# Kernel optimization log

Hardware: AMD Instinct MI355X
Metric: run time of the kernel (lower is better)

## Reference

```python
import jax, jax.numpy as jnp
import numpy as np

N_NODES = 10000
N_EDGES = 640000
D_FEAT = 128


def setup_inputs() -> dict:
    key = jax.random.key(0)
    k1, k2, k3, k4 = jax.random.split(key, 4)
    edge_feat = jax.random.normal(k1, (N_EDGES, D_FEAT), dtype=jnp.float32)
    node_feat = jax.random.normal(k2, (N_NODES, D_FEAT), dtype=jnp.float32)
    recv_idx = jax.random.randint(k3, (N_EDGES,), 0, N_NODES, dtype=jnp.int64 if jax.config.jax_enable_x64 else jnp.int32)
    W = jax.random.normal(k4, (2 * D_FEAT, D_FEAT), dtype=jnp.float32) * (1.0 / np.sqrt(2 * D_FEAT))
    b = jnp.zeros((D_FEAT,), dtype=jnp.float32)
    return {"edge_feat": edge_feat, "node_feat": node_feat, "recv_idx": recv_idx, "W": W, "b": b}


def reference(edge_feat, node_feat, recv_idx, W, b):
    # Unsorted segment sum: scatter-add edge features into receiver nodes. [E,d] -> [N,d]
    n_nodes = node_feat.shape[0]
    agg = jax.ops.segment_sum(edge_feat, recv_idx, num_segments=n_nodes)
    # Concat node features with aggregated received-edge features. [N, 2d]
    collected = jnp.concatenate([node_feat, agg], axis=-1)
    # node_model: Linear(2d -> d)
    return collected @ W + b
```

## Files before the change

kernel.cpp:

```cpp
#include <hip/hip_runtime.h>

#define N_NODES 10000
#define N_EDGES 640000
#define D_FEAT 128

#define WS_COUNTS 0
#define WS_START  16384
#define WS_CURSOR 32768
#define WS_SORTED 49152
#define WS_INTS_NEEDED (WS_SORTED + N_EDGES)

__global__ void zero_counts_kernel(int* __restrict__ counts) {
    int i = blockIdx.x * blockDim.x + threadIdx.x;
    if (i < N_NODES) counts[i] = 0;
}

__global__ void hist_kernel(const int* __restrict__ recv, int* __restrict__ counts) {
    int e = blockIdx.x * blockDim.x + threadIdx.x;
    if (e < N_EDGES) atomicAdd(&counts[recv[e]], 1);
}

__global__ __launch_bounds__(1024) void prefix_kernel(const int* __restrict__ counts,
                                                      int* __restrict__ start,
                                                      int* __restrict__ cursor) {
    __shared__ int wsum[16];
    __shared__ int carry_s;
    const int tid  = threadIdx.x;
    const int lane = tid & 63;
    const int wave = tid >> 6;
    if (tid == 0) carry_s = 0;
    __syncthreads();
    for (int base = 0; base < N_NODES; base += 1024) {
        const int idx = base + tid;
        const int v = (idx < N_NODES) ? counts[idx] : 0;
        int x = v;
        #pragma unroll
        for (int off = 1; off < 64; off <<= 1) {
            int t = __shfl_up(x, off, 64);
            if (lane >= off) x += t;
        }
        if (lane == 63) wsum[wave] = x;
        __syncthreads();
        if (wave == 0) {
            int ws = (lane < 16) ? wsum[lane] : 0;
            #pragma unroll
            for (int off = 1; off < 16; off <<= 1) {
                int t = __shfl_up(ws, off, 64);
                if (lane >= off) ws += t;
            }
            if (lane < 16) wsum[lane] = ws;
        }
        __syncthreads();
        const int carry   = carry_s;
        const int waveoff = (wave == 0) ? 0 : wsum[wave - 1];
        const int excl    = carry + waveoff + x - v;
        if (idx < N_NODES) { start[idx] = excl; cursor[idx] = excl; }
        __syncthreads();
        if (tid == 1023) carry_s = carry + wsum[15];
    }
    if (tid == 0) start[N_NODES] = N_EDGES;
}

__global__ void reorder_kernel(const int* __restrict__ recv,
                               int* __restrict__ cursor,
                               int* __restrict__ sorted_eid) {
    int e = blockIdx.x * blockDim.x + threadIdx.x;
    if (e < N_EDGES) {
        int pos = atomicAdd(&cursor[recv[e]], 1);
        sorted_eid[pos] = e;
    }
}

#define GW 8
__global__ __launch_bounds__(256) void gather_kernel(
        const float4* __restrict__ edge_feat4,
        const int* __restrict__ sorted_eid,
        const int* __restrict__ start,
        float4* __restrict__ agg4) {
    __shared__ float4 red[GW][32];
    const int n   = blockIdx.x;
    const int tid = threadIdx.x;
    const int l   = tid & 31;
    const int w   = tid >> 5;
    const int s = start[n];
    const int e = start[n + 1];
    float4 acc = {0.f, 0.f, 0.f, 0.f};
    for (int i = s + w; i < e; i += GW) {
        const long eid = sorted_eid[i];
        const float4 v = edge_feat4[eid * 32 + l];
        acc.x += v.x; acc.y += v.y; acc.z += v.z; acc.w += v.w;
    }
    red[w][l] = acc;
    __syncthreads();
    if (w == 0) {
        float4 r = red[0][l];
        #pragma unroll
        for (int k = 1; k < GW; ++k) {
            const float4 t = red[k][l];
            r.x += t.x; r.y += t.y; r.z += t.z; r.w += t.w;
        }
        agg4[(long)n * 32 + l] = r;
    }
}

#define NT 16
__global__ __launch_bounds__(128) void gemm_kernel(
        const float* __restrict__ node_feat,
        const float* __restrict__ agg,
        const float* __restrict__ W,
        const float* __restrict__ b,
        float* __restrict__ out) {
    __shared__ float coll[NT][2 * D_FEAT];
    const int n0 = blockIdx.x * NT;
    const int j  = threadIdx.x;

    #pragma unroll
    for (int i = 0; i < NT; ++i) {
        coll[i][j]          = node_feat[(long)(n0 + i) * D_FEAT + j];
        coll[i][D_FEAT + j] = agg[(long)(n0 + i) * D_FEAT + j];
    }
    __syncthreads();

    float acc[NT];
    const float bias = b[j];
    #pragma unroll
    for (int i = 0; i < NT; ++i) acc[i] = bias;

    for (int k = 0; k < 2 * D_FEAT; k += 4) {
        const float w0 = W[(long)(k + 0) * D_FEAT + j];
        const float w1 = W[(long)(k + 1) * D_FEAT + j];
        const float w2 = W[(long)(k + 2) * D_FEAT + j];
        const float w3 = W[(long)(k + 3) * D_FEAT + j];
        #pragma unroll
        for (int i = 0; i < NT; ++i) {
            const float4 c = *(const float4*)&coll[i][k];
            acc[i] += c.x * w0 + c.y * w1 + c.z * w2 + c.w * w3;
        }
    }

    #pragma unroll
    for (int i = 0; i < NT; ++i)
        out[(long)(n0 + i) * D_FEAT + j] = acc[i];
}

extern "C" void kernel_launch(void* const* d_in, const int* in_sizes, int n_in,
                              void* d_out, int out_size, void* d_ws, size_t ws_size,
                              hipStream_t stream) {
    const float* edge_feat = (const float*)d_in[0];
    const float* node_feat = (const float*)d_in[1];
    const int*   recv      = (const int*)d_in[2];
    const float* W         = (const float*)d_in[3];
    const float* b         = (const float*)d_in[4];
    float* out = (float*)d_out;
    float* agg = out;

    int* wsi    = (int*)d_ws;
    int* counts = wsi + WS_COUNTS;
    int* startp = wsi + WS_START;
    int* cursor = wsi + WS_CURSOR;
    int* sorted = wsi + WS_SORTED;

    zero_counts_kernel<<<(N_NODES + 255) / 256, 256, 0, stream>>>(counts);
    hist_kernel<<<(N_EDGES + 255) / 256, 256, 0, stream>>>(recv, counts);
    prefix_kernel<<<1, 1024, 0, stream>>>(counts, startp, cursor);
    reorder_kernel<<<(N_EDGES + 255) / 256, 256, 0, stream>>>(recv, cursor, sorted);
    gather_kernel<<<N_NODES, 256, 0, stream>>>(
        (const float4*)edge_feat, sorted, startp, (float4*)agg);
    gemm_kernel<<<N_NODES / NT, 128, 0, stream>>>(node_feat, agg, W, b, out);
}
```

Baseline: 577.9 us.

## Parallelize prefix scan, vectorize histogram/reorder, prefetch gather, tile GEMM

The single-block prefix scan becomes a three-kernel multi-block scan. Histogram and reorder now read four receiver indices per thread as int4. The gather uses 16 waves per node and prefetches the next sorted edge id while the current row loads. The GEMM becomes a 64x64 register-tiled SGEMM with shared-memory A/B tiles, and agg moves from the output buffer into workspace. These target the serial scan latency and the low-reuse GEMM, at the cost of extra launches and more workspace.

```diff
diff --git a/kernel.cpp b/kernel.cpp
--- a/kernel.cpp
+++ b/kernel.cpp
@@ -5,74 +5,100 @@
 #define D_FEAT 128
 
 #define WS_COUNTS 0
+#define WS_BSUM   10240
+#define WS_BOFF   10304
 #define WS_START  16384
 #define WS_CURSOR 32768
 #define WS_SORTED 49152
-#define WS_INTS_NEEDED (WS_SORTED + N_EDGES)
+#define WS_AGG    689152
+
+#define NPB 40
 
 __global__ void zero_counts_kernel(int* __restrict__ counts) {
     int i = blockIdx.x * blockDim.x + threadIdx.x;
     if (i < N_NODES) counts[i] = 0;
 }
 
-__global__ void hist_kernel(const int* __restrict__ recv, int* __restrict__ counts) {
-    int e = blockIdx.x * blockDim.x + threadIdx.x;
-    if (e < N_EDGES) atomicAdd(&counts[recv[e]], 1);
-}
-
-__global__ __launch_bounds__(1024) void prefix_kernel(const int* __restrict__ counts,
+__global__ void hist_kernel(const int4* __restrict__ recv4, int* __restrict__ counts) {
+    int i = blockIdx.x * blockDim.x + threadIdx.x;
+    if (i < N_EDGES / 4) {
+        const int4 r = recv4[i];
+        atomicAdd(&counts[r.x], 1);
+        atomicAdd(&counts[r.y], 1);
+        atomicAdd(&counts[r.z], 1);
+        atomicAdd(&counts[r.w], 1);
+    }
+}
+
+__global__ __launch_bounds__(256) void prefix1_kernel(const int* __restrict__ counts,
+                                                      int* __restrict__ bsum) {
+    __shared__ int wsum[4];
+    const int tid = threadIdx.x;
+    const int idx = blockIdx.x * 256 + tid;
+    int x = (idx < N_NODES) ? counts[idx] : 0;
+    #pragma unroll
+    for (int off = 32; off >= 1; off >>= 1) x += __shfl_down(x, off, 64);
+    if ((tid & 63) == 0) wsum[tid >> 6] = x;
+    __syncthreads();
+    if (tid == 0) bsum[blockIdx.x] = wsum[0] + wsum[1] + wsum[2] + wsum[3];
+}
+
+__global__ void prefix2_kernel(const int* __restrict__ bsum,
+                               int* __restrict__ boff,
+                               int* __restrict__ start) {
+    const int lane = threadIdx.x;
+    const int v = (lane < NPB) ? bsum[lane] : 0;
+    int x = v;
+    #pragma unroll
+    for (int off = 1; off < 64; off <<= 1) {
+        int t = __shfl_up(x, off, 64);
+        if (lane >= off) x += t;
+    }
+    if (lane < NPB) boff[lane] = x - v;
+    if (lane == 0) start[N_NODES] = N_EDGES;
+}
+
+__global__ __launch_bounds__(256) void prefix3_kernel(const int* __restrict__ counts,
+                                                      const int* __restrict__ boff,
                                                       int* __restrict__ start,
                                                       int* __restrict__ cursor) {
-    __shared__ int wsum[16];
-    __shared__ int carry_s;
+    __shared__ int wsum[4];
     const int tid  = threadIdx.x;
+    const int idx  = blockIdx.x * 256 + tid;
     const int lane = tid & 63;
     const int wave = tid >> 6;
-    if (tid == 0) carry_s = 0;
+    const int v = (idx < N_NODES) ? counts[idx] : 0;
+    int x = v;
+    #pragma unroll
+    for (int off = 1; off < 64; off <<= 1) {
+        int t = __shfl_up(x, off, 64);
+        if (lane >= off) x += t;
+    }
+    if (lane == 63) wsum[wave] = x;
     __syncthreads();
-    for (int base = 0; base < N_NODES; base += 1024) {
-        const int idx = base + tid;
-        const int v = (idx < N_NODES) ? counts[idx] : 0;
-        int x = v;
-        #pragma unroll
-        for (int off = 1; off < 64; off <<= 1) {
-            int t = __shfl_up(x, off, 64);
-            if (lane >= off) x += t;
-        }
-        if (lane == 63) wsum[wave] = x;
-        __syncthreads();
-        if (wave == 0) {
-            int ws = (lane < 16) ? wsum[lane] : 0;
-            #pragma unroll
-            for (int off = 1; off < 16; off <<= 1) {
-                int t = __shfl_up(ws, off, 64);
-                if (lane >= off) ws += t;
-            }
-            if (lane < 16) wsum[lane] = ws;
-        }
-        __syncthreads();
-        const int carry   = carry_s;
-        const int waveoff = (wave == 0) ? 0 : wsum[wave - 1];
-        const int excl    = carry + waveoff + x - v;
-        if (idx < N_NODES) { start[idx] = excl; cursor[idx] = excl; }
-        __syncthreads();
-        if (tid == 1023) carry_s = carry + wsum[15];
-    }
-    if (tid == 0) start[N_NODES] = N_EDGES;
-}
-
-__global__ void reorder_kernel(const int* __restrict__ recv,
+    int woff = 0;
+    #pragma unroll
+    for (int k = 0; k < 3; ++k) woff += (k < wave) ? wsum[k] : 0;
+    const int excl = boff[blockIdx.x] + woff + x - v;
+    if (idx < N_NODES) { start[idx] = excl; cursor[idx] = excl; }
+}
+
+__global__ void reorder_kernel(const int4* __restrict__ recv4,
                                int* __restrict__ cursor,
                                int* __restrict__ sorted_eid) {
-    int e = blockIdx.x * blockDim.x + threadIdx.x;
-    if (e < N_EDGES) {
-        int pos = atomicAdd(&cursor[recv[e]], 1);
-        sorted_eid[pos] = e;
-    }
-}
-
-#define GW 8
-__global__ __launch_bounds__(256) void gather_kernel(
+    int i = blockIdx.x * blockDim.x + threadIdx.x;
+    if (i < N_EDGES / 4) {
+        const int4 r = recv4[i];
+        const int e = i * 4;
+        sorted_eid[atomicAdd(&cursor[r.x], 1)] = e + 0;
+        sorted_eid[atomicAdd(&cursor[r.y], 1)] = e + 1;
+        sorted_eid[atomicAdd(&cursor[r.z], 1)] = e + 2;
+        sorted_eid[atomicAdd(&cursor[r.w], 1)] = e + 3;
+    }
+}
+
+#define GW 16
+__global__ __launch_bounds__(512) void gather_kernel(
         const float4* __restrict__ edge_feat4,
         const int* __restrict__ sorted_eid,
         const int* __restrict__ start,
@@ -85,62 +111,104 @@
     const int s = start[n];
     const int e = start[n + 1];
     float4 acc = {0.f, 0.f, 0.f, 0.f};
-    for (int i = s + w; i < e; i += GW) {
-        const long eid = sorted_eid[i];
-        const float4 v = edge_feat4[eid * 32 + l];
-        acc.x += v.x; acc.y += v.y; acc.z += v.z; acc.w += v.w;
+    int i = s + w;
+    if (i < e) {
+        int eid = sorted_eid[i];
+        while (true) {
+            const int inext = i + GW;
+            const int eid_next = (inext < e) ? sorted_eid[inext] : 0;
+            const float4 v = edge_feat4[(long)eid * 32 + l];
+            acc.x += v.x; acc.y += v.y; acc.z += v.z; acc.w += v.w;
+            i = inext;
+            if (i >= e) break;
+            eid = eid_next;
+        }
     }
     red[w][l] = acc;
     __syncthreads();
     if (w == 0) {
         float4 r = red[0][l];
         #pragma unroll
-        for (int k = 1; k < GW; ++k) {
-            const float4 t = red[k][l];
+        for (int g = 1; g < GW; ++g) {
+            const float4 t = red[g][l];
             r.x += t.x; r.y += t.y; r.z += t.z; r.w += t.w;
         }
         agg4[(long)n * 32 + l] = r;
     }
 }
 
-#define NT 16
-__global__ __launch_bounds__(128) void gemm_kernel(
+__global__ __launch_bounds__(256) void gemm_kernel(
         const float* __restrict__ node_feat,
         const float* __restrict__ agg,
         const float* __restrict__ W,
         const float* __restrict__ b,
         float* __restrict__ out) {
-    __shared__ float coll[NT][2 * D_FEAT];
-    const int n0 = blockIdx.x * NT;
-    const int j  = threadIdx.x;
-
-    #pragma unroll
-    for (int i = 0; i < NT; ++i) {
-        coll[i][j]          = node_feat[(long)(n0 + i) * D_FEAT + j];
-        coll[i][D_FEAT + j] = agg[(long)(n0 + i) * D_FEAT + j];
-    }
-    __syncthreads();
-
-    float acc[NT];
-    const float bias = b[j];
-    #pragma unroll
-    for (int i = 0; i < NT; ++i) acc[i] = bias;
-
-    for (int k = 0; k < 2 * D_FEAT; k += 4) {
-        const float w0 = W[(long)(k + 0) * D_FEAT + j];
-        const float w1 = W[(long)(k + 1) * D_FEAT + j];
-        const float w2 = W[(long)(k + 2) * D_FEAT + j];
-        const float w3 = W[(long)(k + 3) * D_FEAT + j];
+    __shared__ __align__(16) float As[32][68];
+    __shared__ __align__(16) float Bs[32][64];
+    const int tid = threadIdx.x;
+    const int tx = tid & 15;
+    const int ty = tid >> 4;
+    const int m0 = blockIdx.x * 64;
+    const int n0 = blockIdx.y * 64;
+
+    float acc[4][4] = {};
+
+    for (int kt = 0; kt < 2 * D_FEAT; kt += 32) {
+        const float* src = (kt < D_FEAT) ? (node_feat + kt) : (agg + (kt - D_FEAT));
+        {
+            const int r  = tid >> 3;
+            const int c4 = tid & 7;
+            #pragma unroll
+            for (int p = 0; p < 2; ++p) {
+                int row = m0 + p * 32 + r;
+                row = (row < N_NODES) ? row : (N_NODES - 1);
+                const float4 a4 = *(const float4*)(src + (long)row * D_FEAT + c4 * 4);
+                As[c4 * 4 + 0][p * 32 + r] = a4.x;
+                As[c4 * 4 + 1][p * 32 + r] = a4.y;
+                As[c4 * 4 + 2][p * 32 + r] = a4.z;
+                As[c4 * 4 + 3][p * 32 + r] = a4.w;
+            }
+        }
+        {
+            const int r  = tid >> 4;
+            const int c4 = tid & 15;
+            #pragma unroll
+            for (int p = 0; p < 2; ++p) {
+                const int row = kt + p * 16 + r;
+                *(float4*)&Bs[p * 16 + r][c4 * 4] =
+                    *(const float4*)(W + (long)row * D_FEAT + n0 + c4 * 4);
+            }
+        }
+        __syncthreads();
         #pragma unroll
-        for (int i = 0; i < NT; ++i) {
-            const float4 c = *(const float4*)&coll[i][k];
-            acc[i] += c.x * w0 + c.y * w1 + c.z * w2 + c.w * w3;
-        }
-    }
-
-    #pragma unroll
-    for (int i = 0; i < NT; ++i)
-        out[(long)(n0 + i) * D_FEAT + j] = acc[i];
+        for (int kk = 0; kk < 32; ++kk) {
+            const float4 a4 = *(const float4*)&As[kk][ty * 4];
+            const float4 b4 = *(const float4*)&Bs[kk][tx * 4];
+            acc[0][0] += a4.x * b4.x; acc[0][1] += a4.x * b4.y;
+            acc[0][2] += a4.x * b4.z; acc[0][3] += a4.x * b4.w;
+            acc[1][0] += a4.y * b4.x; acc[1][1] += a4.y * b4.y;
+            acc[1][2] += a4.y * b4.z; acc[1][3] += a4.y * b4.w;
+            acc[2][0] += a4.z * b4.x; acc[2][1] += a4.z * b4.y;
+            acc[2][2] += a4.z * b4.z; acc[2][3] += a4.z * b4.w;
+            acc[3][0] += a4.w * b4.x; acc[3][1] += a4.w * b4.y;
+            acc[3][2] += a4.w * b4.z; acc[3][3] += a4.w * b4.w;
+        }
+        __syncthreads();
+    }
+
+    const float4 bias = *(const float4*)(b + n0 + tx * 4);
+    #pragma unroll
+    for (int i2 = 0; i2 < 4; ++i2) {
+        const int row = m0 + ty * 4 + i2;
+        if (row < N_NODES) {
+            float4 o;
+            o.x = acc[i2][0] + bias.x;
+            o.y = acc[i2][1] + bias.y;
+            o.z = acc[i2][2] + bias.z;
+            o.w = acc[i2][3] + bias.w;
+            *(float4*)(out + (long)row * D_FEAT + n0 + tx * 4) = o;
+        }
+    }
 }
 
 extern "C" void kernel_launch(void* const* d_in, const int* in_sizes, int n_in,
@@ -152,19 +220,24 @@
     const float* W         = (const float*)d_in[3];
     const float* b         = (const float*)d_in[4];
     float* out = (float*)d_out;
-    float* agg = out;
 
     int* wsi    = (int*)d_ws;
     int* counts = wsi + WS_COUNTS;
+    int* bsum   = wsi + WS_BSUM;
+    int* boff   = wsi + WS_BOFF;
     int* startp = wsi + WS_START;
     int* cursor = wsi + WS_CURSOR;
     int* sorted = wsi + WS_SORTED;
+    float* agg  = (float*)(wsi + WS_AGG);
 
     zero_counts_kernel<<<(N_NODES + 255) / 256, 256, 0, stream>>>(counts);
-    hist_kernel<<<(N_EDGES + 255) / 256, 256, 0, stream>>>(recv, counts);
-    prefix_kernel<<<1, 1024, 0, stream>>>(counts, startp, cursor);
-    reorder_kernel<<<(N_EDGES + 255) / 256, 256, 0, stream>>>(recv, cursor, sorted);
-    gather_kernel<<<N_NODES, 256, 0, stream>>>(
+    hist_kernel<<<N_EDGES / 4 / 256, 256, 0, stream>>>((const int4*)recv, counts);
+    prefix1_kernel<<<NPB, 256, 0, stream>>>(counts, bsum);
+    prefix2_kernel<<<1, 64, 0, stream>>>(bsum, boff, startp);
+    prefix3_kernel<<<NPB, 256, 0, stream>>>(counts, boff, startp, cursor);
+    reorder_kernel<<<N_EDGES / 4 / 256, 256, 0, stream>>>((const int4*)recv, cursor, sorted);
+    gather_kernel<<<N_NODES, 512, 0, stream>>>(
         (const float4*)edge_feat, sorted, startp, (float4*)agg);
-    gemm_kernel<<<N_NODES / NT, 128, 0, stream>>>(node_feat, agg, W, b, out);
-}
+    dim3 ggrid((N_NODES + 63) / 64, D_FEAT / 64);
+    gemm_kernel<<<ggrid, 256, 0, stream>>>(node_feat, agg, W, b, out);
+}
```

After: 552.3 us. 1.05x faster.
